# Kernel optimization log

Measured on AMD Instinct MI355X. Metric: run time of the kernel, lower is better.

The kernel has to match this reference:

```python
import jax, jax.numpy as jnp
import numpy as np

N_HEAD = 16
NEG_INF = -1e9  # matches the original's -1000000000.0 mask fill


def setup_inputs() -> dict:
    key = jax.random.key(0)
    k1, k2, k3 = jax.random.split(key, 3)
    n_embd = 1024
    b, t = 2, 2048
    x = jax.random.normal(k1, (b, t, n_embd), dtype=jnp.float32)
    w_attn = jax.random.normal(k2, (n_embd, 3 * n_embd), dtype=jnp.float32) * 0.02
    b_attn = jnp.zeros((3 * n_embd,), dtype=jnp.float32)
    w_proj = jax.random.normal(k3, (n_embd, n_embd), dtype=jnp.float32) * 0.02
    b_proj = jnp.zeros((n_embd,), dtype=jnp.float32)
    return {"x": x, "w_attn": w_attn, "b_attn": b_attn, "w_proj": w_proj, "b_proj": b_proj}


def reference(x, w_attn, b_attn, w_proj, b_proj):
    b, t, c = x.shape
    hd = c // N_HEAD
    scale = 1.0 / np.sqrt(hd)
    qkv = x @ w_attn + b_attn                        # [b, t, 3c]
    q, k, v = jnp.split(qkv, 3, axis=-1)
    # split heads -> [b, nh, t, hd]
    def heads(z):
        return z.reshape(b, t, N_HEAD, hd).transpose(0, 2, 1, 3)
    q, k, v = heads(q), heads(k), heads(v)
    att = jnp.einsum('bhqd,bhkd->bhqk', q, k) * scale  # [b, nh, t, t]
    mask = jnp.tril(jnp.ones((t, t), dtype=bool))
    att = jnp.where(mask[None, None], att, jnp.float32(NEG_INF))
    att = jax.nn.softmax(att, axis=-1)
    y = jnp.einsum('bhqk,bhkd->bhqd', att, v)          # [b, nh, t, hd]
    y = y.transpose(0, 2, 1, 3).reshape(b, t, c)
    return y @ w_proj + b_proj
```

## Files before the change

kernel.cpp:

```cpp
#include <hip/hip_runtime.h>
#include <hip/hip_bf16.h>
#include <math.h>

typedef __attribute__((ext_vector_type(8))) short short8;
typedef __attribute__((ext_vector_type(4))) float f32x4;
typedef unsigned short u16;

static __device__ __forceinline__ u16 f2bf(float f) {
  union { float f; unsigned u; } v; v.f = f;
  unsigned r = v.u + 0x7fffu + ((v.u >> 16) & 1u);
  return (u16)(r >> 16);
}

static __device__ __forceinline__ float bf2f(u16 h) {
  union { unsigned u; float f; } v; v.u = ((unsigned)h) << 16;
  return v.f;
}

static __device__ __forceinline__ void gload_lds16(const void* g, void* l) {
  __builtin_amdgcn_global_load_lds(
      (const __attribute__((address_space(1))) void*)g,
      (__attribute__((address_space(3))) void*)l, 16, 0, 0);
}

__device__ __forceinline__ void transpose_tile(const float* __restrict__ W,
                                               u16* __restrict__ WT,
                                               int ND, int KD, int c0, int k0,
                                               float (*tile)[65], int t) {
  const int lr = t >> 2;
  const int lc = (t & 3) * 16;
  const float* src = W + (size_t)(k0 + lr) * ND + c0 + lc;
#pragma unroll
  for (int i = 0; i < 16; i += 4) {
    float4 v = *(const float4*)(src + i);
    tile[lr][lc + i] = v.x; tile[lr][lc + i + 1] = v.y;
    tile[lr][lc + i + 2] = v.z; tile[lr][lc + i + 3] = v.w;
  }
  __syncthreads();
  unsigned pk[8];
#pragma unroll
  for (int j = 0; j < 8; ++j) {
    u16 lo = f2bf(tile[lc + 2 * j][lr]);
    u16 hi = f2bf(tile[lc + 2 * j + 1][lr]);
    pk[j] = lo | ((unsigned)hi << 16);
  }
  u16* dst = WT + (size_t)(c0 + lr) * KD + k0 + lc;
  *(uint4*)(dst) = make_uint4(pk[0], pk[1], pk[2], pk[3]);
  *(uint4*)(dst + 8) = make_uint4(pk[4], pk[5], pk[6], pk[7]);
}

__global__ __launch_bounds__(256) void fused_prologue(const float* __restrict__ x,
                                                      const float* __restrict__ w_attn,
                                                      const float* __restrict__ w_proj,
                                                      u16* __restrict__ xb,
                                                      u16* __restrict__ wTa,
                                                      u16* __restrict__ wTp) {
  __shared__ float tile[64][65];
  const int b = blockIdx.x;
  const int t = threadIdx.x;
  if (b < 2048) {
    const int i = (b * 256 + t) * 8;
    float4 a = *(const float4*)(x + i);
    float4 c = *(const float4*)(x + i + 4);
    uint4 pk;
    pk.x = f2bf(a.x) | ((unsigned)f2bf(a.y) << 16);
    pk.y = f2bf(a.z) | ((unsigned)f2bf(a.w) << 16);
    pk.z = f2bf(c.x) | ((unsigned)f2bf(c.y) << 16);
    pk.w = f2bf(c.z) | ((unsigned)f2bf(c.w) << 16);
    *(uint4*)(xb + i) = pk;
  } else if (b < 2816) {
    const int id = b - 2048;
    transpose_tile(w_attn, wTa, 3072, 1024, (id % 48) * 64, (id / 48) * 64, tile, t);
  } else {
    const int id = b - 2816;
    transpose_tile(w_proj, wTp, 1024, 1024, (id % 16) * 64, (id / 16) * 64, tile, t);
  }
}

template<int NSIZE, int MODE>
__global__ __launch_bounds__(256) void gemm_bt(const u16* __restrict__ A,
                                               const u16* __restrict__ Bt,
                                               const float* __restrict__ bias,
                                               u16* __restrict__ qb,
                                               u16* __restrict__ kb,
                                               u16* __restrict__ vb,
                                               float* __restrict__ outp) {
  constexpr int K = 1024;
  __shared__ u16 As[128 * 128];
  __shared__ u16 Bs[128 * 128];
  const int tid = threadIdx.x;
  const int lane = tid & 63;
  const int wid = tid >> 6;
  const int l15 = lane & 15;
  const int g4 = lane >> 4;
  const int wm = (wid >> 1) * 64;
  const int wn = (wid & 1) * 64;
  const int row0 = blockIdx.x * 128;
  const int col0 = blockIdx.y * 128;

  f32x4 acc[4][4] = {};

  for (int kt = 0; kt < K / 128; ++kt) {
#pragma unroll
    for (int cc = 0; cc < 8; ++cc) {
      const int c = tid + cc * 256;
      const int row = c >> 4;
      const int ch = (c & 15) ^ (row & 15);
      gload_lds16(A + (size_t)(row0 + row) * K + kt * 128 + ch * 8, As + c * 8);
      gload_lds16(Bt + (size_t)(col0 + row) * K + kt * 128 + ch * 8, Bs + c * 8);
    }
    asm volatile("s_waitcnt vmcnt(0)" ::: "memory");
    __builtin_amdgcn_s_barrier();
    asm volatile("" ::: "memory");

#pragma unroll
    for (int ks = 0; ks < 4; ++ks) {
      short8 af[4], bf[4];
#pragma unroll
      for (int mt = 0; mt < 4; ++mt) {
        const int row = wm + mt * 16 + l15;
        af[mt] = *(const short8*)((const char*)As + row * 256 + ((((ks * 4 + g4) ^ l15) & 15) << 4));
      }
#pragma unroll
      for (int nt = 0; nt < 4; ++nt) {
        const int row = wn + nt * 16 + l15;
        bf[nt] = *(const short8*)((const char*)Bs + row * 256 + ((((ks * 4 + g4) ^ l15) & 15) << 4));
      }
#pragma unroll
      for (int mt = 0; mt < 4; ++mt)
#pragma unroll
        for (int nt = 0; nt < 4; ++nt)
          acc[mt][nt] = __builtin_amdgcn_mfma_f32_16x16x32_bf16(af[mt], bf[nt], acc[mt][nt], 0, 0, 0);
    }

    asm volatile("" ::: "memory");
    __builtin_amdgcn_s_barrier();
  }

#pragma unroll
  for (int nt = 0; nt < 4; ++nt) {
    const int col = col0 + wn + nt * 16 + l15;
    const float bv = bias[col];
    if (MODE == 0) {
      const int part = col >> 10;
      const int h = (col >> 6) & 15;
      const int d = col & 63;
      u16* dp = part == 0 ? qb : kb;
#pragma unroll
      for (int mt = 0; mt < 4; ++mt) {
        if (part == 2) {
          const int t0 = row0 + wm + mt * 16 + g4 * 4;
          const int bidx = t0 >> 11;
          const int tt = t0 & 2047;
          const unsigned lo = f2bf(acc[mt][nt][0] + bv) | ((unsigned)f2bf(acc[mt][nt][1] + bv) << 16);
          const unsigned hi = f2bf(acc[mt][nt][2] + bv) | ((unsigned)f2bf(acc[mt][nt][3] + bv) << 16);
          *(uint2*)&vb[((size_t)((bidx << 4) + h) * 64 + d) * 2048 + tt] = make_uint2(lo, hi);
        } else {
#pragma unroll
          for (int r = 0; r < 4; ++r) {
            const int row = row0 + wm + mt * 16 + g4 * 4 + r;
            const int bidx = row >> 11;
            const int tt = row & 2047;
            dp[((size_t)((bidx << 4) + h) * 2048 + tt) * 64 + d] = f2bf(acc[mt][nt][r] + bv);
          }
        }
      }
    } else {
#pragma unroll
      for (int mt = 0; mt < 4; ++mt) {
#pragma unroll
        for (int r = 0; r < 4; ++r) {
          const int row = row0 + wm + mt * 16 + g4 * 4 + r;
          outp[(size_t)row * NSIZE + col] = acc[mt][nt][r] + bv;
        }
      }
    }
  }
}

__global__ __launch_bounds__(256, 3) void attn_fwd(const u16* __restrict__ Qb,
                                                   const u16* __restrict__ Kb,
                                                   const u16* __restrict__ Vtb,
                                                   u16* __restrict__ Yb,
                                                   char* __restrict__ pb) {
  __shared__ u16 Ks[2][64 * 64];
  __shared__ u16 Vs[2][64 * 64];
  __shared__ u16 Ps[4][2048];
  const int bh = blockIdx.x;
  const int y = blockIdx.y;
  int j, c0t, c1t, chunk, split;
  if (y < 8)       { j = 8 + y;  c0t = 0;  c1t = 15;        chunk = 0; split = 1; }
  else if (y < 16) { j = 15 - y; c0t = 0;  c1t = 2 * j + 1; chunk = 0; split = 0; }
  else             { j = y - 8;  c0t = 16; c1t = 2 * j + 1; chunk = 1; split = 1; }
  const int q0 = j * 128;
  const int tid = threadIdx.x;
  const int lane = tid & 63;
  const int wid = tid >> 6;
  const int l15 = lane & 15;
  const int g4 = lane >> 4;
  const size_t bhq = (size_t)bh * 2048 * 64;
  const u16* Kbase = Kb + bhq;
  const u16* Vbase = Vtb + bhq;
  const float C2 = 0.18033688011112042f;
  u16* Pw = &Ps[wid][0];
  const int wrow0 = q0 + wid * 32;

  short8 ones;
#pragma unroll
  for (int i = 0; i < 8; ++i) ones[i] = (short)0x3F80;

  short8 qf[2][2];
#pragma unroll
  for (int g = 0; g < 2; ++g) {
    const u16* qp = Qb + bhq + (size_t)(wrow0 + g * 16 + l15) * 64 + g4 * 8;
    qf[g][0] = *(const short8*)(qp);
    qf[g][1] = *(const short8*)(qp + 32);
  }
  f32x4 accy[2][4] = {};
  float m_q[2] = {-1e30f, -1e30f};
  float m_r[2][4] = {{-1e30f, -1e30f, -1e30f, -1e30f}, {-1e30f, -1e30f, -1e30f, -1e30f}};
  float l_r[2][4] = {};

  int cur = 0;
#pragma unroll
  for (int cc = 0; cc < 2; ++cc) {
    const int c = tid + cc * 256;
    const int srow = c >> 3;
    const int sblk = (c & 7) ^ (srow & 7);
    gload_lds16(Kbase + (size_t)(c0t * 64 + srow) * 64 + sblk * 8, Ks[0] + c * 8);
    gload_lds16(Vbase + (size_t)srow * 2048 + c0t * 64 + sblk * 8, Vs[0] + c * 8);
  }

  for (int kv = c0t; kv <= c1t; ++kv) {
    const int kv0 = kv * 64;
    if (kv < c1t) {
      const int nx0 = kv0 + 64;
#pragma unroll
      for (int cc = 0; cc < 2; ++cc) {
        const int c = tid + cc * 256;
        const int srow = c >> 3;
        const int sblk = (c & 7) ^ (srow & 7);
        gload_lds16(Kbase + (size_t)(nx0 + srow) * 64 + sblk * 8, Ks[cur ^ 1] + c * 8);
        gload_lds16(Vbase + (size_t)srow * 2048 + nx0 + sblk * 8, Vs[cur ^ 1] + c * 8);
      }
      asm volatile("s_waitcnt vmcnt(4)" ::: "memory");
    } else {
      asm volatile("s_waitcnt vmcnt(0)" ::: "memory");
    }
    __builtin_amdgcn_s_barrier();
    asm volatile("" ::: "memory");

    if (kv0 <= wrow0 + 31) {
      const u16* Kt = Ks[cur];
      const u16* Vt = Vs[cur];

      f32x4 s[2][4];
#pragma unroll
      for (int nt = 0; nt < 4; ++nt) {
        const int R = nt * 16 + l15;
        const int sw = (R & 7) << 4;
        short8 kf0 = *(const short8*)((const char*)Kt + R * 128 + ((g4 * 16) ^ sw));
        short8 kf1 = *(const short8*)((const char*)Kt + R * 128 + ((64 + g4 * 16) ^ sw));
        f32x4 z0 = __builtin_amdgcn_mfma_f32_16x16x32_bf16(kf0, qf[0][0], f32x4{}, 0, 0, 0);
        s[0][nt] = __builtin_amdgcn_mfma_f32_16x16x32_bf16(kf1, qf[0][1], z0, 0, 0, 0);
        f32x4 z1 = __builtin_amdgcn_mfma_f32_16x16x32_bf16(kf0, qf[1][0], f32x4{}, 0, 0, 0);
        s[1][nt] = __builtin_amdgcn_mfma_f32_16x16x32_bf16(kf1, qf[1][1], z1, 0, 0, 0);
      }

#pragma unroll
      for (int g = 0; g < 2; ++g) {
        const int grow0 = wrow0 + g * 16;
        if (kv0 + 63 > grow0) {
          const int qg = grow0 + l15;
#pragma unroll
          for (int nt = 0; nt < 4; ++nt) {
            const int kbase = kv0 + nt * 16 + g4 * 4;
#pragma unroll
            for (int r = 0; r < 4; ++r)
              if (kbase + r > qg) s[g][nt][r] = -1e30f;
          }
        }
        float mx = fmaxf(fmaxf(fmaxf(s[g][0][0], s[g][0][1]), fmaxf(s[g][0][2], s[g][0][3])),
                         fmaxf(fmaxf(s[g][1][0], s[g][1][1]), fmaxf(s[g][1][2], s[g][1][3])));
        mx = fmaxf(mx, fmaxf(fmaxf(fmaxf(s[g][2][0], s[g][2][1]), fmaxf(s[g][2][2], s[g][2][3])),
                             fmaxf(fmaxf(s[g][3][0], s[g][3][1]), fmaxf(s[g][3][2], s[g][3][3]))));
        mx = fmaxf(mx, __shfl_xor(mx, 16));
        mx = fmaxf(mx, __shfl_xor(mx, 32));
        if (!__all(mx <= m_q[g] + 44.0f)) {
          m_q[g] = fmaxf(m_q[g], mx);
#pragma unroll
          for (int rr = 0; rr < 4; ++rr) {
            const float mn = __shfl(m_q[g], g4 * 4 + rr);
            const float al = __builtin_amdgcn_exp2f((m_r[g][rr] - mn) * C2);
            m_r[g][rr] = mn;
            l_r[g][rr] *= al;
#pragma unroll
            for (int nt = 0; nt < 4; ++nt) accy[g][nt][rr] *= al;
          }
        }
        const float m2 = m_q[g] * C2;
#pragma unroll
        for (int nt = 0; nt < 4; ++nt)
#pragma unroll
          for (int r = 0; r < 4; ++r)
            s[g][nt][r] = __builtin_amdgcn_exp2f(fmaf(s[g][nt][r], C2, -m2));

#pragma unroll
        for (int nt = 0; nt < 4; ++nt) {
          const unsigned lo = f2bf(s[g][nt][0]) | ((unsigned)f2bf(s[g][nt][1]) << 16);
          const unsigned hi = f2bf(s[g][nt][2]) | ((unsigned)f2bf(s[g][nt][3]) << 16);
          const int rowL = g * 16 + l15;
          const int colB = nt * 32 + g4 * 8;
          *(uint2*)((char*)Pw + rowL * 128 + (colB ^ ((rowL & 7) << 4))) = make_uint2(lo, hi);
        }
      }

      short8 pf[2][2];
#pragma unroll
      for (int g = 0; g < 2; ++g) {
        const int rowL = g * 16 + l15;
        const int sw = (rowL & 7) << 4;
        pf[g][0] = *(const short8*)((const char*)Pw + rowL * 128 + ((g4 * 16) ^ sw));
        pf[g][1] = *(const short8*)((const char*)Pw + rowL * 128 + ((64 + g4 * 16) ^ sw));
      }
#pragma unroll
      for (int g = 0; g < 2; ++g) {
        f32x4 ps = __builtin_amdgcn_mfma_f32_16x16x32_bf16(pf[g][0], ones, f32x4{}, 0, 0, 0);
        ps = __builtin_amdgcn_mfma_f32_16x16x32_bf16(pf[g][1], ones, ps, 0, 0, 0);
#pragma unroll
        for (int rr = 0; rr < 4; ++rr) l_r[g][rr] += ps[rr];
      }
#pragma unroll
      for (int nt = 0; nt < 4; ++nt) {
        const int R = nt * 16 + l15;
        const int sw = (R & 7) << 4;
        short8 vf0 = *(const short8*)((const char*)Vt + R * 128 + ((g4 * 16) ^ sw));
        short8 vf1 = *(const short8*)((const char*)Vt + R * 128 + ((64 + g4 * 16) ^ sw));
#pragma unroll
        for (int g = 0; g < 2; ++g) {
          accy[g][nt] = __builtin_amdgcn_mfma_f32_16x16x32_bf16(pf[g][0], vf0, accy[g][nt], 0, 0, 0);
          accy[g][nt] = __builtin_amdgcn_mfma_f32_16x16x32_bf16(pf[g][1], vf1, accy[g][nt], 0, 0, 0);
        }
      }
    }

    asm volatile("" ::: "memory");
    __builtin_amdgcn_s_barrier();
    cur ^= 1;
  }

  if (!split) {
#pragma unroll
    for (int g = 0; g < 2; ++g)
#pragma unroll
      for (int r = 0; r < 4; ++r) {
        const int row = wrow0 + g * 16 + g4 * 4 + r;
        const float inv = 1.0f / l_r[g][r];
        const size_t base = ((size_t)(bh >> 4) * 2048 + row) * 1024 + (bh & 15) * 64;
#pragma unroll
        for (int nt = 0; nt < 4; ++nt)
          Yb[base + nt * 16 + l15] = f2bf(accy[g][nt][r] * inv);
      }
  } else {
    char* slot = pb + ((size_t)(bh * 8 + (j - 8)) * 2 + chunk) * 17408;
    u16* O = (u16*)slot;
    float* mf = (float*)(slot + 16384);
    float* lf = (float*)(slot + 16896);
#pragma unroll
    for (int g = 0; g < 2; ++g)
#pragma unroll
      for (int r = 0; r < 4; ++r) {
        const int row = wid * 32 + g * 16 + g4 * 4 + r;
        const float inv = 1.0f / l_r[g][r];
#pragma unroll
        for (int nt = 0; nt < 4; ++nt)
          O[row * 64 + nt * 16 + l15] = f2bf(accy[g][nt][r] * inv);
        if (l15 == 0) { mf[row] = m_r[g][r]; lf[row] = l_r[g][r]; }
      }
  }
}

__global__ __launch_bounds__(256) void attn_combine(const char* __restrict__ pb,
                                                    u16* __restrict__ Yb) {
  const int x = blockIdx.x;
  const int bh = blockIdx.y;
  const int j = 8 + (x >> 1);
  const int half = x & 1;
  const int T = 2 * j + half;
  const char* s0 = pb + ((size_t)(bh * 8 + (j - 8)) * 2) * 17408;
  const char* s1 = s0 + 17408;
  const int tid = threadIdx.x;
  const int r64 = tid >> 2;
  const int rowl = half * 64 + r64;
  const int dc = (tid & 3) * 16;
  const float C2 = 0.18033688011112042f;
  const float m0 = ((const float*)(s0 + 16384))[rowl];
  const float m1 = ((const float*)(s1 + 16384))[rowl];
  const float l0 = ((const float*)(s0 + 16896))[rowl];
  const float l1 = ((const float*)(s1 + 16896))[rowl];
  const float m = fmaxf(m0, m1);
  const float w0 = __builtin_amdgcn_exp2f((m0 - m) * C2) * l0;
  const float w1 = __builtin_amdgcn_exp2f((m1 - m) * C2) * l1;
  const float inv = 1.0f / (w0 + w1);
  const float a0 = w0 * inv, a1 = w1 * inv;
  const u16* O0 = (const u16*)s0 + rowl * 64 + dc;
  const u16* O1 = (const u16*)s1 + rowl * 64 + dc;
  const int qrow = T * 64 + r64;
  u16* yp = Yb + ((size_t)(bh >> 4) * 2048 + qrow) * 1024 + (bh & 15) * 64 + dc;
  union { uint4 v; u16 h[8]; } a[2], b[2], o[2];
  a[0].v = *(const uint4*)O0; a[1].v = *(const uint4*)(O0 + 8);
  b[0].v = *(const uint4*)O1; b[1].v = *(const uint4*)(O1 + 8);
#pragma unroll
  for (int jj = 0; jj < 2; ++jj)
#pragma unroll
    for (int i = 0; i < 8; ++i)
      o[jj].h[i] = f2bf(bf2f(a[jj].h[i]) * a0 + bf2f(b[jj].h[i]) * a1);
  *(uint4*)yp = o[0].v;
  *(uint4*)(yp + 8) = o[1].v;
}

extern "C" void kernel_launch(void* const* d_in, const int* in_sizes, int n_in,
                              void* d_out, int out_size, void* d_ws, size_t ws_size,
                              hipStream_t stream) {
  const float* x      = (const float*)d_in[0];
  const float* w_attn = (const float*)d_in[1];
  const float* b_attn = (const float*)d_in[2];
  const float* w_proj = (const float*)d_in[3];
  const float* b_proj = (const float*)d_in[4];
  float* out = (float*)d_out;
  char* ws = (char*)d_ws;

  u16* xb  = (u16*)(ws + (size_t)0);
  u16* wTa = (u16*)(ws + ((size_t)8  << 20));
  u16* wTp = (u16*)(ws + ((size_t)14 << 20));
  u16* qb  = (u16*)(ws + ((size_t)16 << 20));
  u16* kb  = (u16*)(ws + ((size_t)24 << 20));
  u16* vb  = (u16*)(ws + ((size_t)32 << 20));
  u16* yb  = (u16*)(ws + ((size_t)40 << 20));
  char* pb = ws;

  fused_prologue<<<3072, 256, 0, stream>>>(x, w_attn, w_proj, xb, wTa, wTp);
  gemm_bt<3072, 0><<<dim3(32, 24), 256, 0, stream>>>(xb, wTa, b_attn, qb, kb, vb, nullptr);
  attn_fwd<<<dim3(32, 24), 256, 0, stream>>>(qb, kb, vb, yb, pb);
  attn_combine<<<dim3(16, 32), 256, 0, stream>>>(pb, yb);
  gemm_bt<1024, 1><<<dim3(32, 8), 256, 0, stream>>>(yb, wTp, b_proj, nullptr, nullptr, nullptr, out);
}
```

Baseline: 113.8 us.

## Halve P scratch in LDS, use packed bf16 convert, raise occupancy to four

The attention kernel now writes and reads back each 16-row P group right away, reusing one half-size LDS scratch per wave. That shrinks shared memory enough to raise the launch-bounds occupancy hint from 3 to 4 blocks. Manual round-to-nearest bf16 packing is replaced with the hardware v_cvt_pk_bf16_f32 instruction, and the row-max reduction is rewritten as a linear chain. The higher occupancy target may force register spills, and reusing the scratch serialises the two groups through LDS.

```diff
diff --git a/kernel.cpp b/kernel.cpp
--- a/kernel.cpp
+++ b/kernel.cpp
@@ -15,6 +15,12 @@
 static __device__ __forceinline__ float bf2f(u16 h) {
   union { unsigned u; float f; } v; v.u = ((unsigned)h) << 16;
   return v.f;
+}
+
+static __device__ __forceinline__ unsigned cvt_pk_bf16(float lo, float hi) {
+  unsigned r;
+  asm("v_cvt_pk_bf16_f32 %0, %1, %2" : "=v"(r) : "v"(lo), "v"(hi));
+  return r;
 }
 
 static __device__ __forceinline__ void gload_lds16(const void* g, void* l) {
@@ -178,14 +184,14 @@
   }
 }
 
-__global__ __launch_bounds__(256, 3) void attn_fwd(const u16* __restrict__ Qb,
+__global__ __launch_bounds__(256, 4) void attn_fwd(const u16* __restrict__ Qb,
                                                    const u16* __restrict__ Kb,
                                                    const u16* __restrict__ Vtb,
                                                    u16* __restrict__ Yb,
                                                    char* __restrict__ pb) {
   __shared__ u16 Ks[2][64 * 64];
   __shared__ u16 Vs[2][64 * 64];
-  __shared__ u16 Ps[4][2048];
+  __shared__ u16 Ps[4][1024];
   const int bh = blockIdx.x;
   const int y = blockIdx.y;
   int j, c0t, c1t, chunk, split;
@@ -267,6 +273,7 @@
         s[1][nt] = __builtin_amdgcn_mfma_f32_16x16x32_bf16(kf1, qf[1][1], z1, 0, 0, 0);
       }
 
+      short8 pf[2][2];
 #pragma unroll
       for (int g = 0; g < 2; ++g) {
         const int grow0 = wrow0 + g * 16;
@@ -280,10 +287,14 @@
               if (kbase + r > qg) s[g][nt][r] = -1e30f;
           }
         }
-        float mx = fmaxf(fmaxf(fmaxf(s[g][0][0], s[g][0][1]), fmaxf(s[g][0][2], s[g][0][3])),
-                         fmaxf(fmaxf(s[g][1][0], s[g][1][1]), fmaxf(s[g][1][2], s[g][1][3])));
-        mx = fmaxf(mx, fmaxf(fmaxf(fmaxf(s[g][2][0], s[g][2][1]), fmaxf(s[g][2][2], s[g][2][3])),
-                             fmaxf(fmaxf(s[g][3][0], s[g][3][1]), fmaxf(s[g][3][2], s[g][3][3]))));
+        float mx = fmaxf(s[g][0][0], s[g][0][1]);
+        mx = fmaxf(fmaxf(mx, s[g][0][2]), s[g][0][3]);
+        mx = fmaxf(fmaxf(mx, s[g][1][0]), s[g][1][1]);
+        mx = fmaxf(fmaxf(mx, s[g][1][2]), s[g][1][3]);
+        mx = fmaxf(fmaxf(mx, s[g][2][0]), s[g][2][1]);
+        mx = fmaxf(fmaxf(mx, s[g][2][2]), s[g][2][3]);
+        mx = fmaxf(fmaxf(mx, s[g][3][0]), s[g][3][1]);
+        mx = fmaxf(fmaxf(mx, s[g][3][2]), s[g][3][3]);
         mx = fmaxf(mx, __shfl_xor(mx, 16));
         mx = fmaxf(mx, __shfl_xor(mx, 32));
         if (!__all(mx <= m_q[g] + 44.0f)) {
@@ -307,22 +318,18 @@
 
 #pragma unroll
         for (int nt = 0; nt < 4; ++nt) {
-          const unsigned lo = f2bf(s[g][nt][0]) | ((unsigned)f2bf(s[g][nt][1]) << 16);
-          const unsigned hi = f2bf(s[g][nt][2]) | ((unsigned)f2bf(s[g][nt][3]) << 16);
-          const int rowL = g * 16 + l15;
+          const unsigned lo = cvt_pk_bf16(s[g][nt][0], s[g][nt][1]);
+          const unsigned hi = cvt_pk_bf16(s[g][nt][2], s[g][nt][3]);
           const int colB = nt * 32 + g4 * 8;
-          *(uint2*)((char*)Pw + rowL * 128 + (colB ^ ((rowL & 7) << 4))) = make_uint2(lo, hi);
-        }
-      }
-
-      short8 pf[2][2];
-#pragma unroll
-      for (int g = 0; g < 2; ++g) {
-        const int rowL = g * 16 + l15;
-        const int sw = (rowL & 7) << 4;
-        pf[g][0] = *(const short8*)((const char*)Pw + rowL * 128 + ((g4 * 16) ^ sw));
-        pf[g][1] = *(const short8*)((const char*)Pw + rowL * 128 + ((64 + g4 * 16) ^ sw));
-      }
+          *(uint2*)((char*)Pw + l15 * 128 + (colB ^ ((l15 & 7) << 4))) = make_uint2(lo, hi);
+        }
+        {
+          const int sw = (l15 & 7) << 4;
+          pf[g][0] = *(const short8*)((const char*)Pw + l15 * 128 + ((g4 * 16) ^ sw));
+          pf[g][1] = *(const short8*)((const char*)Pw + l15 * 128 + ((64 + g4 * 16) ^ sw));
+        }
+      }
+
 #pragma unroll
       for (int g = 0; g < 2; ++g) {
         f32x4 ps = __builtin_amdgcn_mfma_f32_16x16x32_bf16(pf[g][0], ones, f32x4{}, 0, 0, 0);
```

Measured after the change: 136.9 us. +20.3%, slower.
